# Kernel tuning notes

Measured on AMD Instinct MI355X. Metric: run time of the kernel, lower is better.

The kernel has to match this reference:

```python
import jax, jax.numpy as jnp
import numpy as np

H, D = 8, 64
LN_EPS = 1e-5

def elu_p1(x):
    return jax.nn.elu(x) + 1.0

def sum_norm(x):
    return x / jnp.sum(x, axis=-1, keepdims=True)

def setup_inputs() -> dict:
    key = jax.random.key(0)
    k1, k2, k3 = jax.random.split(key, 3)
    slen, bsz, in_dim = 1024, 32, 512
    x = jax.random.normal(k1, (slen, bsz, in_dim), dtype=jnp.float32)
    ln_gamma = jnp.ones((in_dim,), dtype=jnp.float32)
    ln_beta = jnp.zeros((in_dim,), dtype=jnp.float32)
    # Linear weights stored as [in, out] (transposed vs torch) and fan-in scaled
    w_slow = jax.random.normal(k2, (in_dim, H * (3 * D + 1)), dtype=jnp.float32) / np.sqrt(in_dim)
    w_out = jax.random.normal(k3, (H * D, in_dim), dtype=jnp.float32) / np.sqrt(H * D)
    return {"x": x, "ln_gamma": ln_gamma, "ln_beta": ln_beta, "w_slow": w_slow, "w_out": w_out}

def reference(x, ln_gamma, ln_beta, w_slow, w_out):
    slen, bsz, in_dim = x.shape
    # LayerNorm
    mu = jnp.mean(x, axis=-1, keepdims=True)
    var = jnp.mean((x - mu) ** 2, axis=-1, keepdims=True)
    h = (x - mu) * jax.lax.rsqrt(var + LN_EPS) * ln_gamma + ln_beta
    # slow net projection -> q, k, v, beta per head
    qkvb = (h @ w_slow).reshape(slen, bsz, H, 3 * D + 1)
    q, k, v, beta = jnp.split(qkvb, [D, 2 * D, 3 * D], axis=-1)
    beta = jax.nn.sigmoid(beta)            # [slen, bsz, H, 1]
    q = sum_norm(elu_p1(q))                # [slen, bsz, H, D]
    k = sum_norm(elu_p1(k))
    # delta-rule fast-weight recurrence over time
    W0 = jnp.zeros((bsz, H, D, D), dtype=x.dtype)
    def step(W, inp):
        q_t, k_t, v_t, b_t = inp           # [bsz,H,D], [bsz,H,D], [bsz,H,D], [bsz,H,1]
        v_old = jnp.einsum('bhij,bhj->bhi', W, k_t)
        upd = b_t * (v_t - v_old)          # [bsz,H,D]
        W = W + upd[..., :, None] * k_t[..., None, :]
        o_t = jnp.einsum('bhij,bhj->bhi', W, q_t)
        return W, o_t
    _, outs = jax.lax.scan(step, W0, (q, k, v, beta))  # outs [slen, bsz, H, D]
    out = outs.reshape(slen, bsz, H * D) @ w_out       # [slen, bsz, in_dim]
    return x + out
```

## Files before the change

kernel.cpp:

```cpp
#include <hip/hip_runtime.h>
#include <cstdint>

using short8  = __attribute__((ext_vector_type(8))) short;
using ushort8 = __attribute__((ext_vector_type(8))) unsigned short;
using short4v = __attribute__((ext_vector_type(4))) short;
using f32x4   = __attribute__((ext_vector_type(4))) float;

#define H_    8
#define SLEN  1024
#define BSZ   32
#define INDIM 512
#define NQKV  1544
#define NPAD2 1792
#define MROWS 32768
#define PB    72

#define GLOAD16(gp, lp) __builtin_amdgcn_global_load_lds( \
    (const __attribute__((address_space(1))) void*)(gp),  \
    (__attribute__((address_space(3))) void*)(lp), 16, 0, 0)

#define VMCNT8() do { asm volatile("s_waitcnt vmcnt(8)" ::: "memory"); \
                      __builtin_amdgcn_sched_barrier(0); } while (0)
#define VMCNT0() do { asm volatile("s_waitcnt vmcnt(0)" ::: "memory"); \
                      __builtin_amdgcn_sched_barrier(0); } while (0)
#define SBAR()   do { __builtin_amdgcn_sched_barrier(0); \
                      __builtin_amdgcn_s_barrier(); \
                      __builtin_amdgcn_sched_barrier(0); } while (0)

static __device__ __forceinline__ float bf2f(unsigned short s) {
    return __uint_as_float(((unsigned int)s) << 16);
}
#if defined(__BF16_MANT_DIG__)
static __device__ __forceinline__ unsigned short f2bf(float f) {
    union { __bf16 b; unsigned short u; } cv;
    cv.b = (__bf16)f;
    return cv.u;
}
#else
static __device__ __forceinline__ unsigned short f2bf(float f) {
    unsigned int u = __float_as_uint(f);
    u += 0x7FFFu + ((u >> 16) & 1u);
    return (unsigned short)(u >> 16);
}
#endif

__global__ __launch_bounds__(256) void ln_kernel(const float* __restrict__ x,
                                                 const float* __restrict__ gamma,
                                                 const float* __restrict__ betap,
                                                 unsigned short* __restrict__ h) {
    int row = blockIdx.x * 4 + (threadIdx.x >> 6);
    int l   = threadIdx.x & 63;
    const f32x4* xr = (const f32x4*)(x + (size_t)row * INDIM);
    f32x4 a = xr[l * 2], b = xr[l * 2 + 1];
    float s = 0.f, sq = 0.f;
    #pragma unroll
    for (int j = 0; j < 4; ++j) { s += a[j]; sq += a[j] * a[j]; }
    #pragma unroll
    for (int j = 0; j < 4; ++j) { s += b[j]; sq += b[j] * b[j]; }
    #pragma unroll
    for (int off = 32; off; off >>= 1) { s += __shfl_xor(s, off); sq += __shfl_xor(sq, off); }
    float mean = s * (1.f / 512.f);
    float var  = sq * (1.f / 512.f) - mean * mean;
    float rstd = rsqrtf(var + 1e-5f);
    const f32x4* g4 = (const f32x4*)gamma;
    const f32x4* b4 = (const f32x4*)betap;
    f32x4 g0 = g4[l * 2], g1 = g4[l * 2 + 1], e0 = b4[l * 2], e1 = b4[l * 2 + 1];
    short8 o;
    #pragma unroll
    for (int j = 0; j < 4; ++j) o[j]     = (short)f2bf((a[j] - mean) * rstd * g0[j] + e0[j]);
    #pragma unroll
    for (int j = 0; j < 4; ++j) o[4 + j] = (short)f2bf((b[j] - mean) * rstd * g1[j] + e1[j]);
    ((short8*)(h + (size_t)row * INDIM))[l] = o;
}

__global__ __launch_bounds__(256) void cvt_wslow(const float* __restrict__ w,
                                                 unsigned short* __restrict__ wT) {
    int idx = blockIdx.x * 256 + threadIdx.x;
    int n = idx >> 9, k = idx & 511;
    int c;
    if (n < 512)       c = (n >> 6) * 193 + (n & 63);
    else if (n < 1024) c = ((n - 512) >> 6) * 193 + 64 + (n & 63);
    else if (n < 1536) c = ((n - 1024) >> 6) * 193 + 128 + (n & 63);
    else if (n < 1544) c = (n - 1536) * 193 + 192;
    else               c = -1;
    wT[idx] = (c >= 0) ? f2bf(w[(size_t)k * NQKV + c]) : (unsigned short)0;
}
__global__ __launch_bounds__(256) void cvt_wout(const float* __restrict__ w,
                                                unsigned short* __restrict__ wT) {
    int idx = blockIdx.x * 256 + threadIdx.x;
    int n = idx >> 9, k = idx & 511;
    wT[idx] = f2bf(w[(size_t)k * 512 + n]);
}

__global__ __launch_bounds__(512, 2) void gemm_qkv(const unsigned short* __restrict__ A,
                                                   const unsigned short* __restrict__ BT,
                                                   unsigned short* __restrict__ qn,
                                                   unsigned short* __restrict__ kn,
                                                   unsigned short* __restrict__ vn,
                                                   float* __restrict__ bet) {
    __shared__ unsigned short As[2][256 * 64];
    __shared__ unsigned short Bs[2][256 * 64];
    const int tid = threadIdx.x;
    const int id = blockIdx.y * 7 + blockIdx.x;
    const int newid = (id & 7) * 112 + (id >> 3);
    const int bx = newid % 7;
    const int n0 = bx * 256;
    const int m0 = (newid / 7) * 256;
    const int w = tid >> 6, l = tid & 63;
    const int wm = w >> 2, wn = w & 3;
    const int lr = l & 15, lk8 = (l >> 4) * 8;
    f32x4 acc[8][4] = {};

    auto STAGE = [&](int buf, int kt) {
        #pragma unroll
        for (int c2 = 0; c2 < 4; ++c2) {
            int idx = c2 * 512 + tid;
            int row = idx >> 3, kc2 = (idx & 7) * 8;
            int lb = (c2 * 512 + (tid & 448)) * 8;
            GLOAD16(A  + (size_t)(m0 + row) * INDIM + kt + kc2, &As[buf][lb]);
            GLOAD16(BT + (size_t)(n0 + row) * INDIM + kt + kc2, &Bs[buf][lb]);
        }
    };
    auto COMPUTE = [&](int buf) {
        short8 bf2[4][2];
        #pragma unroll
        for (int ni = 0; ni < 4; ++ni)
            #pragma unroll
            for (int kk = 0; kk < 2; ++kk)
                bf2[ni][kk] = *(const short8*)&Bs[buf][(wn * 64 + ni * 16 + lr) * 64 + kk * 32 + lk8];
        #pragma unroll
        for (int p = 0; p < 4; ++p) {
            short8 af[2][2];
            #pragma unroll
            for (int d = 0; d < 2; ++d)
                #pragma unroll
                for (int kk = 0; kk < 2; ++kk)
                    af[d][kk] = *(const short8*)&As[buf][(wm * 128 + (2 * p + d) * 16 + lr) * 64 + kk * 32 + lk8];
            #pragma unroll
            for (int d = 0; d < 2; ++d)
                #pragma unroll
                for (int ni = 0; ni < 4; ++ni)
                    #pragma unroll
                    for (int kk = 0; kk < 2; ++kk)
                        acc[2 * p + d][ni] =
                            __builtin_amdgcn_mfma_f32_16x16x32_bf16(af[d][kk], bf2[ni][kk], acc[2 * p + d][ni], 0, 0, 0);
        }
    };

    STAGE(0, 0);
    STAGE(1, 64);
    #pragma unroll
    for (int tp = 0; tp < 4; ++tp) {
        VMCNT8();
        SBAR();
        COMPUTE(0);
        SBAR();
        if (tp < 3) {
            STAGE(0, (2 * tp + 2) * 64);
            VMCNT8();
        } else {
            VMCNT0();
        }
        SBAR();
        COMPUTE(1);
        SBAR();
        if (tp < 3) STAGE(1, (2 * tp + 3) * 64);
    }

    const int g = l >> 4, cc = l & 15;
    const int colbase = n0 + wn * 64;
    if (bx < 6) {
        const int reg  = colbase >> 9;
        const int head = (colbase >> 6) & 7;
        unsigned short* dst = (reg == 0) ? qn : (reg == 1) ? kn : vn;
        #pragma unroll
        for (int mi = 0; mi < 8; ++mi) {
            #pragma unroll
            for (int j = 0; j < 4; ++j) {
                int row = m0 + wm * 128 + mi * 16 + g * 4 + j;
                int s = row >> 5, b = row & 31;
                size_t base = ((size_t)(b * H_ + head) * SLEN + s) * 64;
                float e0 = acc[mi][0][j], e1 = acc[mi][1][j], e2 = acc[mi][2][j], e3 = acc[mi][3][j];
                if (reg < 2) {
                    e0 = e0 > 0.f ? e0 + 1.f : __expf(e0);
                    e1 = e1 > 0.f ? e1 + 1.f : __expf(e1);
                    e2 = e2 > 0.f ? e2 + 1.f : __expf(e2);
                    e3 = e3 > 0.f ? e3 + 1.f : __expf(e3);
                    float ssum = (e0 + e1) + (e2 + e3);
                    ssum += __shfl_xor(ssum, 1);
                    ssum += __shfl_xor(ssum, 2);
                    ssum += __shfl_xor(ssum, 4);
                    ssum += __shfl_xor(ssum, 8);
                    float inv = 1.f / ssum;
                    e0 *= inv; e1 *= inv; e2 *= inv; e3 *= inv;
                }
                dst[base +  0 + cc] = f2bf(e0);
                dst[base + 16 + cc] = f2bf(e1);
                dst[base + 32 + cc] = f2bf(e2);
                dst[base + 48 + cc] = f2bf(e3);
            }
        }
    } else {
        if (wn == 0 && cc < 8) {
            #pragma unroll
            for (int mi = 0; mi < 8; ++mi)
                #pragma unroll
                for (int j = 0; j < 4; ++j) {
                    int row = m0 + wm * 128 + mi * 16 + g * 4 + j;
                    int s = row >> 5, b = row & 31;
                    float v = acc[mi][0][j];
                    bet[(size_t)(b * H_ + cc) * SLEN + s] = 1.f / (1.f + __expf(-v));
                }
        }
    }
}

__global__ __launch_bounds__(256) void gemm_out(const unsigned short* __restrict__ A,
                                                const unsigned short* __restrict__ BT,
                                                const float* __restrict__ X,
                                                float* __restrict__ outf) {
    __shared__ unsigned short As[128 * 64];
    __shared__ unsigned short Bs[128 * 64];
    const int t  = threadIdx.x;
    const int id = blockIdx.y * 4 + blockIdx.x;
    const int newid = (id & 7) * 128 + (id >> 3);
    const int n0 = (newid % 4) * 128;
    const int m0 = (newid / 4) * 128;
    const int w = t >> 6, l = t & 63;
    const int wr = (w >> 1) * 64, wc = (w & 1) * 64;
    f32x4 acc[4][4] = {};
    for (int kt = 0; kt < INDIM; kt += 64) {
        __syncthreads();
        #pragma unroll
        for (int c = 0; c < 4; ++c) {
            int idx = c * 256 + t;
            int row = idx >> 3, kc2 = (idx & 7) * 8;
            int lb = (c * 256 + (t & 192)) * 8;
            GLOAD16(A  + (size_t)(m0 + row) * INDIM + kt + kc2, &As[lb]);
            GLOAD16(BT + (size_t)(n0 + row) * INDIM + kt + kc2, &Bs[lb]);
        }
        __syncthreads();
        #pragma unroll
        for (int kk = 0; kk < 2; ++kk) {
            const int kr = kk * 32 + (l >> 4) * 8;
            short8 af[4], bf[4];
            #pragma unroll
            for (int m = 0; m < 4; ++m) af[m] = *(const short8*)&As[(wr + m * 16 + (l & 15)) * 64 + kr];
            #pragma unroll
            for (int n = 0; n < 4; ++n) bf[n] = *(const short8*)&Bs[(wc + n * 16 + (l & 15)) * 64 + kr];
            #pragma unroll
            for (int m = 0; m < 4; ++m)
                #pragma unroll
                for (int n = 0; n < 4; ++n)
                    acc[m][n] = __builtin_amdgcn_mfma_f32_16x16x32_bf16(af[m], bf[n], acc[m][n], 0, 0, 0);
        }
    }
    const int rb = (l >> 4) * 4, cc = l & 15;
    #pragma unroll
    for (int m = 0; m < 4; ++m)
        #pragma unroll
        for (int n = 0; n < 4; ++n)
            #pragma unroll
            for (int j = 0; j < 4; ++j) {
                int row = m0 + wr + m * 16 + rb + j;
                int col = n0 + wc + n * 16 + cc;
                size_t o = (size_t)row * 512 + col;
                outf[o] = X[o] + acc[m][n][j];
            }
}

__global__ __launch_bounds__(512, 4) void fwtiles(const unsigned short* __restrict__ qn,
                                                  const unsigned short* __restrict__ kn,
                                                  const unsigned short* __restrict__ vn,
                                                  const float* __restrict__ beta,
                                                  unsigned short* __restrict__ tiles,
                                                  unsigned short* __restrict__ outs) {
    __shared__ unsigned short Ax[64 * PB], Atr[64 * PB], Pw[64 * PB], Pwtr[64 * PB];
    __shared__ unsigned short Z0[128 * PB], Z1[128 * PB];
    __shared__ float bv[64];
    const int bx = blockIdx.x;
    const int bh = bx >> 4, c = bx & 15;
    const int b = bh >> 3, h = bh & 7;
    const int c0 = c * 64;
    const int tid = threadIdx.x;
    const int w = tid >> 6, l = tid & 63;
    const int mw = w & 3, nh = w >> 2;
    const int lr = l & 15, lk = (l >> 4) << 3, rb = (l >> 4) << 2;
    const unsigned short* kc = kn + ((size_t)bh * SLEN + c0) * 64;
    const unsigned short* qc = qn + ((size_t)bh * SLEN + c0) * 64;
    const unsigned short* vc = vn + ((size_t)bh * SLEN + c0) * 64;
    const float* bb = beta + (size_t)bh * SLEN + c0;

    {
        #pragma unroll
        for (int i = 0; i < 2; ++i) {
            int idx = i * 512 + tid;
            int row = idx >> 3, seg = idx & 7;
            const unsigned short* src = (row < 64) ? (vc + (size_t)row * 64 + seg * 8)
                                                   : (kc + (size_t)(row - 64) * 64 + seg * 8);
            *(ushort8*)&Z1[row * PB + seg * 8] = *(const ushort8*)src;
        }
        if (tid < 64) bv[tid] = bb[tid];
        ushort8 z8 = {};
        for (int i = tid; i < 576; i += 512) { ((ushort8*)Ax)[i] = z8; ((ushort8*)Atr)[i] = z8; }
    }
    __syncthreads();

    auto ldb = [&](const unsigned short* M, int m, int kk) -> short8 {
        return *(const short8*)&M[(m * 16 + lr) * PB + kk * 32 + lk];
    };

    {
        const int zoff2 = (w >> 2) * 64;
        const int tbase = (w & 3) * 16;
        const float sgn = (w >= 4) ? -1.f : 1.f;
        ushort8 b0v, b1v;
        #pragma unroll
        for (int i = 0; i < 16; ++i) {
            int r = w * 16 + i;
            float val = sgn * bv[tbase + i] * bf2f(Z1[r * PB + l]);
            unsigned short uv = f2bf(val);
            if (i < 8) b0v[i] = uv; else b1v[i - 8] = uv;
        }
        *(ushort8*)&Z0[(zoff2 + l) * PB + tbase]     = b0v;
        *(ushort8*)&Z0[(zoff2 + l) * PB + tbase + 8] = b1v;
    }
    {
        const int pm[10] = {0, 1, 1, 2, 2, 2, 3, 3, 3, 3};
        const int pn[10] = {0, 0, 1, 0, 1, 2, 0, 1, 2, 3};
        for (int pi = w; pi < 10; pi += 8) {
            int m = pm[pi], n = pn[pi];
            short8 ka0 = *(const short8*)&Z1[(64 + 16 * m + lr) * PB + lk];
            short8 ka1 = *(const short8*)&Z1[(64 + 16 * m + lr) * PB + 32 + lk];
            short8 kb0 = *(const short8*)&Z1[(64 + 16 * n + lr) * PB + lk];
            short8 kb1 = *(const short8*)&Z1[(64 + 16 * n + lr) * PB + 32 + lk];
            f32x4 a = {};
            a = __builtin_amdgcn_mfma_f32_16x16x32_bf16(ka0, kb0, a, 0, 0, 0);
            a = __builtin_amdgcn_mfma_f32_16x16x32_bf16(ka1, kb1, a, 0, 0, 0);
            f32x4 btm = *(const f32x4*)&bv[16 * m + rb];
            short4v pk;
            #pragma unroll
            for (int j = 0; j < 4; ++j) {
                int tt = 16 * m + rb + j, s = 16 * n + lr;
                unsigned short v = (s < tt) ? f2bf(-btm[j] * a[j]) : (unsigned short)0;
                Ax[tt * PB + s] = v;
                pk[j] = (short)v;
            }
            *(short4v*)&Atr[(16 * n + lr) * PB + 16 * m + rb] = pk;
        }
    }
    __syncthreads();

    auto zprod = [&](const unsigned short* Xb, int p, const unsigned short* Zs, unsigned short* Zd) {
        const bool msk0 = (16 * mw + 15 >= p), msk1 = (16 * mw + 15 - 32 >= p);
        short8 xf0, xf1;
        if (msk0) xf0 = ldb(Xb, mw, 0);
        if (msk1) xf1 = ldb(Xb, mw, 1);
        #pragma unroll
        for (int ni = 0; ni < 4; ++ni) {
            int n = nh * 4 + ni;
            short4v zi = *(const short4v*)&Zs[(16 * n + lr) * PB + 16 * mw + rb];
            f32x4 a;
            #pragma unroll
            for (int j = 0; j < 4; ++j) a[j] = bf2f((unsigned short)zi[j]);
            if (msk0) a = __builtin_amdgcn_mfma_f32_16x16x32_bf16(xf0, ldb(Zs, n, 0), a, 0, 0, 0);
            if (msk1) a = __builtin_amdgcn_mfma_f32_16x16x32_bf16(xf1, ldb(Zs, n, 1), a, 0, 0, 0);
            short4v zo;
            #pragma unroll
            for (int j = 0; j < 4; ++j) zo[j] = (short)f2bf(a[j]);
            *(short4v*)&Zd[(16 * n + lr) * PB + 16 * mw + rb] = zo;
        }
    };
    auto powp = [&](const unsigned short* Ps, const unsigned short* Pstr, int p,
                    unsigned short* Pd, unsigned short* Pdtr) {
        const bool x0 = (16 * mw + 15 >= p), x1 = (16 * mw + 15 - 32 >= p);
        short8 xf0, xf1;
        if (x0) xf0 = ldb(Ps, mw, 0);
        if (x1) xf1 = ldb(Ps, mw, 1);
        #pragma unroll
        for (int ni = 0; ni < 2; ++ni) {
            int n = nh * 2 + ni;
            const bool y0 = (31 - 16 * n >= p), y1 = (63 - 16 * n >= p);
            f32x4 a = {};
            if (x0 && y0) a = __builtin_amdgcn_mfma_f32_16x16x32_bf16(xf0, ldb(Pstr, n, 0), a, 0, 0, 0);
            if (x1 && y1) a = __builtin_amdgcn_mfma_f32_16x16x32_bf16(xf1, ldb(Pstr, n, 1), a, 0, 0, 0);
            short4v pk;
            #pragma unroll
            for (int j = 0; j < 4; ++j) {
                unsigned short v = f2bf(a[j]);
                Pd[(16 * mw + rb + j) * PB + 16 * n + lr] = v;
                pk[j] = (short)v;
            }
            *(short4v*)&Pdtr[(16 * n + lr) * PB + 16 * mw + rb] = pk;
        }
    };

    zprod(Ax, 1, Z0, Z1);  powp(Ax, Atr, 1, Pw, Pwtr);  __syncthreads();
    zprod(Pw, 2, Z1, Z0);  powp(Pw, Pwtr, 2, Ax, Atr);  __syncthreads();
    zprod(Ax, 4, Z0, Z1);  powp(Ax, Atr, 4, Pw, Pwtr);  __syncthreads();
    zprod(Pw, 8, Z1, Z0);  powp(Pw, Pwtr, 8, Ax, Atr);  __syncthreads();
    zprod(Ax, 16, Z0, Z1); powp(Ax, Atr, 16, Pw, Pwtr); __syncthreads();
    zprod(Pw, 32, Z1, Z0);
    __syncthreads();

    {
        #pragma unroll
        for (int i = 0; i < 2; ++i) {
            int idx = i * 512 + tid;
            int row = idx >> 3, seg = idx & 7;
            const unsigned short* src = (row < 64) ? (qc + (size_t)row * 64 + seg * 8)
                                                   : (kc + (size_t)(row - 64) * 64 + seg * 8);
            *(ushort8*)&Z1[row * PB + seg * 8] = *(const ushort8*)src;
        }
    }
    __syncthreads();

    {
        short8 qa0 = *(const short8*)&Z1[(16 * mw + lr) * PB + lk];
        short8 qa1 = *(const short8*)&Z1[(16 * mw + lr) * PB + 32 + lk];
        #pragma unroll
        for (int ni = 0; ni < 2; ++ni) {
            int n = nh * 2 + ni;
            short8 kb0 = *(const short8*)&Z1[(64 + 16 * n + lr) * PB + lk];
            short8 kb1 = *(const short8*)&Z1[(64 + 16 * n + lr) * PB + 32 + lk];
            f32x4 a = {};
            a = __builtin_amdgcn_mfma_f32_16x16x32_bf16(qa0, kb0, a, 0, 0, 0);
            a = __builtin_amdgcn_mfma_f32_16x16x32_bf16(qa1, kb1, a, 0, 0, 0);
            #pragma unroll
            for (int j = 0; j < 4; ++j) {
                int tt = 16 * mw + rb + j, s = 16 * n + lr;
                Ax[tt * PB + s] = (s <= tt) ? f2bf(a[j]) : (unsigned short)0;
            }
        }
        ushort8 kv;
        #pragma unroll
        for (int j = 0; j < 8; ++j)
            kv[j] = Z1[(64 + w * 8 + j) * PB + l];
        *(ushort8*)&Pwtr[l * PB + w * 8] = kv;
    }
    __syncthreads();

    {
        unsigned short* tb = tiles + ((size_t)bh * 16 + c) * 12288;
        short8 pA0 = ldb(Ax, mw, 0), pA1 = ldb(Ax, mw, 1);
        short8 zA0 = ldb(Z0, mw, 0), zA1 = ldb(Z0, mw, 1);
        short8 kt0 = ldb(Pwtr, mw, 0), kt1 = ldb(Pwtr, mw, 1);
        #pragma unroll
        for (int ni = 0; ni < 2; ++ni) {
            int n = nh * 2 + ni;
            f32x4 aN = {};
            aN = __builtin_amdgcn_mfma_f32_16x16x32_bf16(zA0, ldb(Pwtr, n, 0), aN, 0, 0, 0);
            aN = __builtin_amdgcn_mfma_f32_16x16x32_bf16(zA1, ldb(Pwtr, n, 1), aN, 0, 0, 0);
            f32x4 aM = {};
            aM = __builtin_amdgcn_mfma_f32_16x16x32_bf16(kt0, ldb(Z0, 4 + n, 0), aM, 0, 0, 0);
            aM = __builtin_amdgcn_mfma_f32_16x16x32_bf16(kt1, ldb(Z0, 4 + n, 1), aM, 0, 0, 0);
            f32x4 aG;
            #pragma unroll
            for (int j = 0; j < 4; ++j) aG[j] = bf2f(Z1[(16 * mw + rb + j) * PB + 16 * n + lr]);
            aG = __builtin_amdgcn_mfma_f32_16x16x32_bf16(pA0, ldb(Z0, 4 + n, 0), aG, 0, 0, 0);
            aG = __builtin_amdgcn_mfma_f32_16x16x32_bf16(pA1, ldb(Z0, 4 + n, 1), aG, 0, 0, 0);
            f32x4 aP = {};
            aP = __builtin_amdgcn_mfma_f32_16x16x32_bf16(pA0, ldb(Z0, n, 0), aP, 0, 0, 0);
            aP = __builtin_amdgcn_mfma_f32_16x16x32_bf16(pA1, ldb(Z0, n, 1), aP, 0, 0, 0);
            #pragma unroll
            for (int j = 0; j < 4; ++j) {
                int r = 16 * mw + rb + j, cl = 16 * n + lr;
                tb[r * 64 + cl]        = f2bf(aM[j]);
                tb[4096 + r * 64 + cl] = f2bf(aG[j]);
                tb[8192 + r * 64 + cl] = f2bf(aN[j]);
                outs[((size_t)(c0 + r) * BSZ + b) * 512 + h * 64 + cl] = f2bf(aP[j]);
            }
        }
    }
}

__global__ __launch_bounds__(256) void fwscan_w(const unsigned short* __restrict__ tiles,
                                                unsigned short* __restrict__ wchk) {
    __shared__ float Wf[64 * 68];
    const int bh = blockIdx.x;
    const int tid = threadIdx.x;
    const int w = tid >> 6, l = tid & 63;
    const int lr = l & 15, lk = (l >> 4) << 3, rb = (l >> 4) << 2;
    const int cr = l >> 3, cc8 = (l & 7) * 8;
    #pragma unroll
    for (int j = 0; j < 16; ++j) Wf[(16 * w + j) * 68 + l] = 0.f;

    const unsigned short* tb0 = tiles + (size_t)bh * 16 * 12288;
    unsigned short* wc0 = wchk + (size_t)bh * 16 * 4096;

    auto loadc = [&](short8 (&MT)[4][2], unsigned short (&NV)[4][4], int c) {
        const unsigned short* tb = tb0 + (size_t)c * 12288;
        #pragma unroll
        for (int n = 0; n < 4; ++n) {
            MT[n][0] = *(const short8*)(tb + (size_t)(16 * n + lr) * 64 + lk);
            MT[n][1] = *(const short8*)(tb + (size_t)(16 * n + lr) * 64 + 32 + lk);
            #pragma unroll
            for (int j = 0; j < 4; ++j)
                NV[n][j] = tb[8192 + (size_t)(16 * w + rb + j) * 64 + 16 * n + lr];
        }
    };
    auto stepc = [&](short8 (&MT)[4][2], unsigned short (&NV)[4][4], int c) {
        #pragma unroll
        for (int half = 0; half < 2; ++half) {
            int row = 16 * w + half * 8 + cr;
            const float* p = &Wf[row * 68 + cc8];
            f32x4 x0 = *(const f32x4*)p, x1 = *(const f32x4*)(p + 4);
            ushort8 o;
            #pragma unroll
            for (int j = 0; j < 4; ++j) { o[j] = f2bf(x0[j]); o[4 + j] = f2bf(x1[j]); }
            *(ushort8*)(wc0 + (size_t)c * 4096 + row * 64 + cc8) = o;
        }
        short8 wf0, wf1;
        {
            const float* p0 = &Wf[(16 * w + lr) * 68 + lk];
            f32x4 a0 = *(const f32x4*)p0, b0 = *(const f32x4*)(p0 + 4);
            f32x4 a1 = *(const f32x4*)(p0 + 32), b1 = *(const f32x4*)(p0 + 36);
            #pragma unroll
            for (int j = 0; j < 4; ++j) {
                wf0[j] = (short)f2bf(a0[j]); wf0[4 + j] = (short)f2bf(b0[j]);
                wf1[j] = (short)f2bf(a1[j]); wf1[4 + j] = (short)f2bf(b1[j]);
            }
        }
        #pragma unroll
        for (int n = 0; n < 4; ++n) {
            f32x4 a;
            #pragma unroll
            for (int j = 0; j < 4; ++j)
                a[j] = Wf[(16 * w + rb + j) * 68 + 16 * n + lr] + bf2f(NV[n][j]);
            a = __builtin_amdgcn_mfma_f32_16x16x32_bf16(wf0, MT[n][0], a, 0, 0, 0);
            a = __builtin_amdgcn_mfma_f32_16x16x32_bf16(wf1, MT[n][1], a, 0, 0, 0);
            #pragma unroll
            for (int j = 0; j < 4; ++j) Wf[(16 * w + rb + j) * 68 + 16 * n + lr] = a[j];
        }
    };

    short8 mtA[4][2], mtB[4][2];
    unsigned short nvA[4][4], nvB[4][4];
    loadc(mtA, nvA, 0);
    #pragma unroll 1
    for (int cc = 0; cc < 8; ++cc) {
        int c = 2 * cc;
        if (c + 1 < 16) loadc(mtB, nvB, c + 1);
        stepc(mtA, nvA, c);
        if (c + 2 < 16) loadc(mtA, nvA, c + 2);
        stepc(mtB, nvB, c + 1);
    }
}

__global__ __launch_bounds__(256) void fw_o(const unsigned short* __restrict__ tiles,
                                            const unsigned short* __restrict__ wchk,
                                            unsigned short* __restrict__ outs) {
    __shared__ unsigned short Ot[64 * 72];
    const int c = blockIdx.x + 1;
    const int bh = blockIdx.y;
    const int b = bh >> 3, h = bh & 7;
    const int c0 = c * 64;
    const int tid = threadIdx.x;
    const int w = tid >> 6, l = tid & 63;
    const int lr = l & 15, lk = (l >> 4) << 3, rb = (l >> 4) << 2;
    const unsigned short* G  = tiles + ((size_t)bh * 16 + c) * 12288 + 4096;
    const unsigned short* W0 = wchk + ((size_t)bh * 16 + c) * 4096;

    #pragma unroll
    for (int i = 0; i < 2; ++i) {
        int idx = i * 256 + tid;
        int t = idx >> 3, d0 = (idx & 7) * 8;
        *(ushort8*)&Ot[t * 72 + d0] =
            *(const ushort8*)(outs + ((size_t)(c0 + t) * BSZ + b) * 512 + h * 64 + d0);
    }
    __syncthreads();

    short8 g0 = *(const short8*)(G + (size_t)(16 * w + lr) * 64 + lk);
    short8 g1 = *(const short8*)(G + (size_t)(16 * w + lr) * 64 + 32 + lk);
    #pragma unroll
    for (int n = 0; n < 4; ++n) {
        short8 wf0 = *(const short8*)(W0 + (size_t)(16 * n + lr) * 64 + lk);
        short8 wf1 = *(const short8*)(W0 + (size_t)(16 * n + lr) * 64 + 32 + lk);
        f32x4 a;
        #pragma unroll
        for (int j = 0; j < 4; ++j) a[j] = bf2f(Ot[(16 * w + rb + j) * 72 + 16 * n + lr]);
        a = __builtin_amdgcn_mfma_f32_16x16x32_bf16(g0, wf0, a, 0, 0, 0);
        a = __builtin_amdgcn_mfma_f32_16x16x32_bf16(g1, wf1, a, 0, 0, 0);
        #pragma unroll
        for (int j = 0; j < 4; ++j) Ot[(16 * w + rb + j) * 72 + 16 * n + lr] = f2bf(a[j]);
    }
    __syncthreads();

    #pragma unroll
    for (int i = 0; i < 2; ++i) {
        int idx = i * 256 + tid;
        int t = idx >> 3, d0 = (idx & 7) * 8;
        *(ushort8*)(outs + ((size_t)(c0 + t) * BSZ + b) * 512 + h * 64 + d0) =
            *(const ushort8*)&Ot[t * 72 + d0];
    }
}

extern "C" void kernel_launch(void* const* d_in, const int* in_sizes, int n_in,
                              void* d_out, int out_size, void* d_ws, size_t ws_size,
                              hipStream_t stream) {
    const float* x      = (const float*)d_in[0];
    const float* g      = (const float*)d_in[1];
    const float* be     = (const float*)d_in[2];
    const float* w_slow = (const float*)d_in[3];
    const float* w_out  = (const float*)d_in[4];
    float* out = (float*)d_out;
    char* ws = (char*)d_ws;

    unsigned short* h    = (unsigned short*)(ws);
    unsigned short* outs = (unsigned short*)(ws);
    unsigned short* qn   = (unsigned short*)(ws + 33554432);
    unsigned short* wchk = (unsigned short*)(ws + 33554432);
    unsigned short* kn   = (unsigned short*)(ws + 67108864);
    unsigned short* vn   = (unsigned short*)(ws + 100663296);
    float*          bet  = (float*)         (ws + 134217728);
    unsigned short* wsT  = (unsigned short*)(ws + 135266304);
    unsigned short* woT  = (unsigned short*)(ws + 137101312);
    unsigned short* tiles= (unsigned short*)(ws + 137625600);

    if (ws_size < 238288896) return;

    ln_kernel<<<8192, 256, 0, stream>>>(x, g, be, h);
    cvt_wslow<<<(NPAD2 * 512) / 256, 256, 0, stream>>>(w_slow, wsT);
    cvt_wout<<<(512 * 512) / 256, 256, 0, stream>>>(w_out, woT);
    gemm_qkv<<<dim3(7, MROWS / 256), 512, 0, stream>>>(h, wsT, qn, kn, vn, bet);
    fwtiles<<<BSZ * H_ * 16, 512, 0, stream>>>(qn, kn, vn, bet, tiles, outs);
    fwscan_w<<<BSZ * H_, 256, 0, stream>>>(tiles, wchk);
    fw_o<<<dim3(15, BSZ * H_), 256, 0, stream>>>(tiles, wchk, outs);
    gemm_out<<<dim3(4, MROWS / 128), 256, 0, stream>>>(outs, woT, x, out);
}
```

Measured before the change: 339.6 us.

## Double-buffer output GEMM with larger 256x256 tiles; skip unused transpose write

```diff
diff --git a/kernel.cpp b/kernel.cpp
--- a/kernel.cpp
+++ b/kernel.cpp
@@ -215,57 +215,89 @@
     }
 }
 
-__global__ __launch_bounds__(256) void gemm_out(const unsigned short* __restrict__ A,
-                                                const unsigned short* __restrict__ BT,
-                                                const float* __restrict__ X,
-                                                float* __restrict__ outf) {
-    __shared__ unsigned short As[128 * 64];
-    __shared__ unsigned short Bs[128 * 64];
-    const int t  = threadIdx.x;
-    const int id = blockIdx.y * 4 + blockIdx.x;
-    const int newid = (id & 7) * 128 + (id >> 3);
-    const int n0 = (newid % 4) * 128;
-    const int m0 = (newid / 4) * 128;
-    const int w = t >> 6, l = t & 63;
-    const int wr = (w >> 1) * 64, wc = (w & 1) * 64;
-    f32x4 acc[4][4] = {};
-    for (int kt = 0; kt < INDIM; kt += 64) {
-        __syncthreads();
-        #pragma unroll
-        for (int c = 0; c < 4; ++c) {
-            int idx = c * 256 + t;
+__global__ __launch_bounds__(512, 2) void gemm_out(const unsigned short* __restrict__ A,
+                                                   const unsigned short* __restrict__ BT,
+                                                   const float* __restrict__ X,
+                                                   float* __restrict__ outf) {
+    __shared__ unsigned short As[2][256 * 64];
+    __shared__ unsigned short Bs[2][256 * 64];
+    const int tid = threadIdx.x;
+    const int id = blockIdx.y * 2 + blockIdx.x;
+    const int newid = (id & 7) * 32 + (id >> 3);
+    const int n0 = (newid & 1) * 256;
+    const int m0 = (newid >> 1) * 256;
+    const int w = tid >> 6, l = tid & 63;
+    const int wm = w >> 2, wn = w & 3;
+    const int lr = l & 15, lk8 = (l >> 4) * 8;
+    f32x4 acc[8][4] = {};
+
+    auto STAGE = [&](int buf, int kt) {
+        #pragma unroll
+        for (int c2 = 0; c2 < 4; ++c2) {
+            int idx = c2 * 512 + tid;
             int row = idx >> 3, kc2 = (idx & 7) * 8;
-            int lb = (c * 256 + (t & 192)) * 8;
-            GLOAD16(A  + (size_t)(m0 + row) * INDIM + kt + kc2, &As[lb]);
-            GLOAD16(BT + (size_t)(n0 + row) * INDIM + kt + kc2, &Bs[lb]);
-        }
-        __syncthreads();
-        #pragma unroll
-        for (int kk = 0; kk < 2; ++kk) {
-            const int kr = kk * 32 + (l >> 4) * 8;
-            short8 af[4], bf[4];
-            #pragma unroll
-            for (int m = 0; m < 4; ++m) af[m] = *(const short8*)&As[(wr + m * 16 + (l & 15)) * 64 + kr];
-            #pragma unroll
-            for (int n = 0; n < 4; ++n) bf[n] = *(const short8*)&Bs[(wc + n * 16 + (l & 15)) * 64 + kr];
-            #pragma unroll
-            for (int m = 0; m < 4; ++m)
+            int lb = (c2 * 512 + (tid & 448)) * 8;
+            GLOAD16(A  + (size_t)(m0 + row) * INDIM + kt + kc2, &As[buf][lb]);
+            GLOAD16(BT + (size_t)(n0 + row) * INDIM + kt + kc2, &Bs[buf][lb]);
+        }
+    };
+    auto COMPUTE = [&](int buf) {
+        short8 bf2[4][2];
+        #pragma unroll
+        for (int ni = 0; ni < 4; ++ni)
+            #pragma unroll
+            for (int kk = 0; kk < 2; ++kk)
+                bf2[ni][kk] = *(const short8*)&Bs[buf][(wn * 64 + ni * 16 + lr) * 64 + kk * 32 + lk8];
+        #pragma unroll
+        for (int p = 0; p < 4; ++p) {
+            short8 af[2][2];
+            #pragma unroll
+            for (int d = 0; d < 2; ++d)
                 #pragma unroll
-                for (int n = 0; n < 4; ++n)
-                    acc[m][n] = __builtin_amdgcn_mfma_f32_16x16x32_bf16(af[m], bf[n], acc[m][n], 0, 0, 0);
-        }
-    }
-    const int rb = (l >> 4) * 4, cc = l & 15;
-    #pragma unroll
-    for (int m = 0; m < 4; ++m)
-        #pragma unroll
-        for (int n = 0; n < 4; ++n)
+                for (int kk = 0; kk < 2; ++kk)
+                    af[d][kk] = *(const short8*)&As[buf][(wm * 128 + (2 * p + d) * 16 + lr) * 64 + kk * 32 + lk8];
+            #pragma unroll
+            for (int d = 0; d < 2; ++d)
+                #pragma unroll
+                for (int ni = 0; ni < 4; ++ni)
+                    #pragma unroll
+                    for (int kk = 0; kk < 2; ++kk)
+                        acc[2 * p + d][ni] =
+                            __builtin_amdgcn_mfma_f32_16x16x32_bf16(af[d][kk], bf2[ni][kk], acc[2 * p + d][ni], 0, 0, 0);
+        }
+    };
+
+    STAGE(0, 0);
+    STAGE(1, 64);
+    #pragma unroll
+    for (int tp = 0; tp < 4; ++tp) {
+        VMCNT8();
+        SBAR();
+        COMPUTE(0);
+        SBAR();
+        if (tp < 3) {
+            STAGE(0, (2 * tp + 2) * 64);
+            VMCNT8();
+        } else {
+            VMCNT0();
+        }
+        SBAR();
+        COMPUTE(1);
+        SBAR();
+        if (tp < 3) STAGE(1, (2 * tp + 3) * 64);
+    }
+
+    const int g = l >> 4, cc = l & 15;
+    #pragma unroll
+    for (int mi = 0; mi < 8; ++mi)
+        #pragma unroll
+        for (int ni = 0; ni < 4; ++ni)
             #pragma unroll
             for (int j = 0; j < 4; ++j) {
-                int row = m0 + wr + m * 16 + rb + j;
-                int col = n0 + wc + n * 16 + cc;
+                int row = m0 + wm * 128 + mi * 16 + g * 4 + j;
+                int col = n0 + wn * 64 + ni * 16 + cc;
                 size_t o = (size_t)row * 512 + col;
-                outf[o] = X[o] + acc[m][n][j];
+                outf[o] = X[o] + acc[mi][ni][j];
             }
 }
 
@@ -372,7 +404,7 @@
         }
     };
     auto powp = [&](const unsigned short* Ps, const unsigned short* Pstr, int p,
-                    unsigned short* Pd, unsigned short* Pdtr) {
+                    unsigned short* Pd, unsigned short* Pdtr, bool wrTr) {
         const bool x0 = (16 * mw + 15 >= p), x1 = (16 * mw + 15 - 32 >= p);
         short8 xf0, xf1;
         if (x0) xf0 = ldb(Ps, mw, 0);
@@ -391,15 +423,15 @@
                 Pd[(16 * mw + rb + j) * PB + 16 * n + lr] = v;
                 pk[j] = (short)v;
             }
-            *(short4v*)&Pdtr[(16 * n + lr) * PB + 16 * mw + rb] = pk;
-        }
-    };
-
-    zprod(Ax, 1, Z0, Z1);  powp(Ax, Atr, 1, Pw, Pwtr);  __syncthreads();
-    zprod(Pw, 2, Z1, Z0);  powp(Pw, Pwtr, 2, Ax, Atr);  __syncthreads();
-    zprod(Ax, 4, Z0, Z1);  powp(Ax, Atr, 4, Pw, Pwtr);  __syncthreads();
-    zprod(Pw, 8, Z1, Z0);  powp(Pw, Pwtr, 8, Ax, Atr);  __syncthreads();
-    zprod(Ax, 16, Z0, Z1); powp(Ax, Atr, 16, Pw, Pwtr); __syncthreads();
+            if (wrTr) *(short4v*)&Pdtr[(16 * n + lr) * PB + 16 * mw + rb] = pk;
+        }
+    };
+
+    zprod(Ax, 1, Z0, Z1);  powp(Ax, Atr, 1, Pw, Pwtr, true);   __syncthreads();
+    zprod(Pw, 2, Z1, Z0);  powp(Pw, Pwtr, 2, Ax, Atr, true);   __syncthreads();
+    zprod(Ax, 4, Z0, Z1);  powp(Ax, Atr, 4, Pw, Pwtr, true);   __syncthreads();
+    zprod(Pw, 8, Z1, Z0);  powp(Pw, Pwtr, 8, Ax, Atr, true);   __syncthreads();
+    zprod(Ax, 16, Z0, Z1); powp(Ax, Atr, 16, Pw, Pwtr, false); __syncthreads();
     zprod(Pw, 32, Z1, Z0);
     __syncthreads();
 
@@ -626,5 +658,5 @@
     fwtiles<<<BSZ * H_ * 16, 512, 0, stream>>>(qn, kn, vn, bet, tiles, outs);
     fwscan_w<<<BSZ * H_, 256, 0, stream>>>(tiles, wchk);
     fw_o<<<dim3(15, BSZ * H_), 256, 0, stream>>>(tiles, wchk, outs);
-    gemm_out<<<dim3(4, MROWS / 128), 256, 0, stream>>>(outs, woT, x, out);
-}
+    gemm_out<<<dim3(2, MROWS / 256), 512, 0, stream>>>(outs, woT, x, out);
+}
```

Measured after the change: 337.5 us. Within noise of the previous version (-0.6%).
